# Kernel tuning notes

Measured on AMD Instinct MI355X. Metric: run time of the kernel, lower is better.

## Reference

```python
import jax, jax.numpy as jnp
import numpy as np

DIM = 768
HEADS = 12
HD = DIM // HEADS  # 64
BASE = 100.0


def rope_sincos(H, W):
    # DINOv3 RopePositionEmbedding: normalize_coords='separate', base=100.0
    dd = HD // 4
    periods = BASE ** (jnp.arange(dd, dtype=jnp.float32) / dd)          # [dd]
    ch = (jnp.arange(H, dtype=jnp.float32) + 0.5) / H                    # pixel centers
    cw = (jnp.arange(W, dtype=jnp.float32) + 0.5) / W
    cy, cx = jnp.meshgrid(ch, cw, indexing='ij')
    coords = 2.0 * jnp.stack([cy, cx], axis=-1).reshape(H * W, 2) - 1.0  # [N,2] in [-1,1]
    angles = 2.0 * jnp.pi * coords[:, :, None] / periods[None, None, :]  # [N,2,dd]
    angles = angles.reshape(H * W, 2 * dd)                               # [N, HD//2]
    angles = jnp.concatenate([angles, angles], axis=-1)                  # [N, HD]
    return jnp.sin(angles), jnp.cos(angles)


def rotate_half(t):
    t1, t2 = jnp.split(t, 2, axis=-1)
    return jnp.concatenate([-t2, t1], axis=-1)


def setup_inputs() -> dict:
    key = jax.random.key(0)
    k1, k2, k3 = jax.random.split(key, 3)
    B, H, W = 2, 48, 48
    x = jax.random.normal(k1, (B, H, W, DIM), dtype=jnp.float32)
    w_qkv = jax.random.normal(k2, (3 * DIM, DIM), dtype=jnp.float32) * 0.02
    b_qkv = jnp.zeros((3 * DIM,), dtype=jnp.float32)
    w_proj = jax.random.normal(k3, (DIM, DIM), dtype=jnp.float32) * 0.02
    b_proj = jnp.zeros((DIM,), dtype=jnp.float32)
    return {"x": x, "w_qkv": w_qkv, "b_qkv": b_qkv, "w_proj": w_proj, "b_proj": b_proj}


def reference(x, w_qkv, b_qkv, w_proj, b_proj):
    B, H, W, C = x.shape
    N = H * W
    xf = x.reshape(B, N, C)
    qkv = xf @ w_qkv.T + b_qkv                                   # [B,N,3C]
    qkv = qkv.reshape(B, N, 3, HEADS, HD).transpose(2, 0, 3, 1, 4)
    q, k, v = qkv[0], qkv[1], qkv[2]                              # [B,h,N,d]
    sin, cos = rope_sincos(H, W)                                  # [N,d]
    q = q * cos + rotate_half(q) * sin
    k = k * cos + rotate_half(k) * sin
    scale = HD ** -0.5
    attn = jax.nn.softmax(jnp.einsum('bhqd,bhkd->bhqk', q, k) * scale, axis=-1)
    o = jnp.einsum('bhqk,bhkd->bhqd', attn, v)                    # [B,h,N,d]
    o = o.transpose(0, 2, 1, 3).reshape(B, N, C)
    o = o @ w_proj.T + b_proj
    return o.reshape(B, H, W, C)
```

## Files before the change

kernel.cpp:

```cpp
#include <hip/hip_runtime.h>

#define BATCH 2
#define NSEQ 2304
#define DIM 768
#define HEADS 12
#define HD 64
#define M_TOK (BATCH * NSEQ)
#define LDSP 72
#define KP 72
#define BH (BATCH * HEADS)
#define KT_HALF (NSEQ / 64 / 2)

typedef __attribute__((ext_vector_type(8))) short bf16x8;
typedef __attribute__((ext_vector_type(8))) short short8v;
typedef __attribute__((ext_vector_type(4))) float f32x4;
typedef __fp16 fp16x2 __attribute__((ext_vector_type(2)));
typedef _Float16 half4 __attribute__((ext_vector_type(4)));
typedef _Float16 half8 __attribute__((ext_vector_type(8)));

#define QSCALE (0.125f * 1.44269504088896f)
#define LOG2_100_D16 0.41524101186092029f

__device__ __forceinline__ short f2bf(float f) {
    union { float f; unsigned u; } v; v.f = f;
    unsigned r = v.u + 0x7fffu + ((v.u >> 16) & 1u);
    return (short)(r >> 16);
}

#define CN1 (M_TOK * DIM / 4)
#define CN2 (3 * DIM * DIM / 4)
#define CN3 (DIM * DIM / 4)
__global__ void cvt_all_kernel(const float* __restrict__ x, const float* __restrict__ wq,
                               const float* __restrict__ wp,
                               short* __restrict__ xb, short* __restrict__ wqb,
                               short* __restrict__ wpb) {
    int i = blockIdx.x * 256 + threadIdx.x;
    const float* src; short* dst; int j;
    if (i < CN1)              { src = x;  dst = xb;  j = i; }
    else if (i < CN1 + CN2)   { src = wq; dst = wqb; j = i - CN1; }
    else                      { src = wp; dst = wpb; j = i - CN1 - CN2; }
    float4 v = reinterpret_cast<const float4*>(src)[j];
    short4 o;
    o.x = f2bf(v.x); o.y = f2bf(v.y); o.z = f2bf(v.z); o.w = f2bf(v.w);
    reinterpret_cast<short4*>(dst)[j] = o;
}

__global__ __launch_bounds__(256) void gemm_qkv_kernel(
    const short* __restrict__ A,
    const short* __restrict__ Bt,
    const float* __restrict__ bias,
    short* __restrict__ qb, short* __restrict__ kbuf, _Float16* __restrict__ vtb)
{
    __shared__ __align__(16) short At[2][128 * LDSP];
    __shared__ __align__(16) short Bl[2][128 * LDSP];
    const int m0 = blockIdx.x * 128, n0 = blockIdx.y * 128;
    const int tid = threadIdx.x, lane = tid & 63, wave = tid >> 6;
    const int quad = lane >> 4, l16 = lane & 15;
    const int wm = (wave >> 1) * 64, wn = (wave & 1) * 64;
    const int r = tid >> 1, c0 = (tid & 1) * 32;
    f32x4 acc[4][4] = {};

    {
        const uint4* ga = reinterpret_cast<const uint4*>(&A[(size_t)(m0 + r) * DIM + c0]);
        const uint4* gb = reinterpret_cast<const uint4*>(&Bt[(size_t)(n0 + r) * DIM + c0]);
        uint4 a0 = ga[0], a1 = ga[1], a2 = ga[2], a3 = ga[3];
        uint4 b0 = gb[0], b1 = gb[1], b2 = gb[2], b3 = gb[3];
        uint4* sa = reinterpret_cast<uint4*>(&At[0][r * LDSP + c0]);
        uint4* sb = reinterpret_cast<uint4*>(&Bl[0][r * LDSP + c0]);
        sa[0] = a0; sa[1] = a1; sa[2] = a2; sa[3] = a3;
        sb[0] = b0; sb[1] = b1; sb[2] = b2; sb[3] = b3;
    }

    int cur = 0;
    for (int k0 = 0; k0 < DIM; k0 += 64) {
        __syncthreads();
        uint4 a0, a1, a2, a3, b0, b1, b2, b3;
        const bool pre = (k0 + 64 < DIM);
        if (pre) {
            const uint4* ga = reinterpret_cast<const uint4*>(&A[(size_t)(m0 + r) * DIM + k0 + 64 + c0]);
            const uint4* gb = reinterpret_cast<const uint4*>(&Bt[(size_t)(n0 + r) * DIM + k0 + 64 + c0]);
            a0 = ga[0]; a1 = ga[1]; a2 = ga[2]; a3 = ga[3];
            b0 = gb[0]; b1 = gb[1]; b2 = gb[2]; b3 = gb[3];
        }
#pragma unroll
        for (int ks = 0; ks < 2; ++ks) {
            bf16x8 af[4], bf[4];
#pragma unroll
            for (int mt = 0; mt < 4; ++mt)
                af[mt] = *reinterpret_cast<const bf16x8*>(&At[cur][(wm + mt * 16 + l16) * LDSP + ks * 32 + quad * 8]);
#pragma unroll
            for (int nt = 0; nt < 4; ++nt)
                bf[nt] = *reinterpret_cast<const bf16x8*>(&Bl[cur][(wn + nt * 16 + l16) * LDSP + ks * 32 + quad * 8]);
#pragma unroll
            for (int mt = 0; mt < 4; ++mt)
#pragma unroll
                for (int nt = 0; nt < 4; ++nt)
                    acc[mt][nt] = __builtin_amdgcn_mfma_f32_16x16x32_bf16(af[mt], bf[nt], acc[mt][nt], 0, 0, 0);
        }
        if (pre) {
            uint4* sa = reinterpret_cast<uint4*>(&At[cur ^ 1][r * LDSP + c0]);
            uint4* sb = reinterpret_cast<uint4*>(&Bl[cur ^ 1][r * LDSP + c0]);
            sa[0] = a0; sa[1] = a1; sa[2] = a2; sa[3] = a3;
            sb[0] = b0; sb[1] = b1; sb[2] = b2; sb[3] = b3;
        }
        cur ^= 1;
    }

    const int which = (n0 + wn) / DIM;
    const int head = ((n0 + wn) % DIM) / HD;
    const int b = m0 / NSEQ;
    const int tokb = m0 % NSEQ + wm;
    if (which == 2) {
#pragma unroll
        for (int mt = 0; mt < 4; ++mt)
#pragma unroll
            for (int nt = 0; nt < 4; ++nt) {
                const int n = n0 + wn + nt * 16 + l16;
                const int d = nt * 16 + l16;
                const float bi = bias[n];
                const int tok0 = tokb + mt * 16 + quad * 4;
                half4 hv;
                hv.x = (_Float16)(acc[mt][nt][0] + bi);
                hv.y = (_Float16)(acc[mt][nt][1] + bi);
                hv.z = (_Float16)(acc[mt][nt][2] + bi);
                hv.w = (_Float16)(acc[mt][nt][3] + bi);
                *reinterpret_cast<half4*>(&vtb[((size_t)(b * HEADS + head) * HD + d) * NSEQ + tok0]) = hv;
            }
    } else {
        short* dst = (which == 0) ? qb : kbuf;
        const float qs = (which == 0) ? QSCALE : 1.0f;
        float bi[4];
#pragma unroll
        for (int nt = 0; nt < 4; ++nt) bi[nt] = bias[n0 + wn + nt * 16 + l16];
        const float invp = __builtin_amdgcn_exp2f(-(float)l16 * LOG2_100_D16);
#pragma unroll
        for (int mt = 0; mt < 4; ++mt) {
#pragma unroll
            for (int rg = 0; rg < 4; ++rg) {
                const int tok = tokb + mt * 16 + quad * 4 + rg;
                const int yy = tok / 48, xx = tok - yy * 48;
                const float ry = (2.0f * (yy + 0.5f) * (1.0f / 48.0f) - 1.0f) * invp;
                const float rx = (2.0f * (xx + 0.5f) * (1.0f / 48.0f) - 1.0f) * invp;
                const float sy = __builtin_amdgcn_sinf(ry), cy = __builtin_amdgcn_cosf(ry);
                const float sx = __builtin_amdgcn_sinf(rx), cx = __builtin_amdgcn_cosf(rx);
                const float a0 = acc[mt][0][rg] + bi[0];
                const float a1 = acc[mt][1][rg] + bi[1];
                const float a2 = acc[mt][2][rg] + bi[2];
                const float a3 = acc[mt][3][rg] + bi[3];
                short* rp = &dst[((size_t)(b * HEADS + head) * NSEQ + tok) * HD];
                rp[l16]      = f2bf((a0 * cy - a2 * sy) * qs);
                rp[32 + l16] = f2bf((a2 * cy + a0 * sy) * qs);
                rp[16 + l16] = f2bf((a1 * cx - a3 * sx) * qs);
                rp[48 + l16] = f2bf((a3 * cx + a1 * sx) * qs);
            }
        }
    }
}

__global__ __launch_bounds__(256, 2) void attn_kernel(
    const short* __restrict__ qb, const short* __restrict__ kb,
    const _Float16* __restrict__ vtb, _Float16* __restrict__ opart,
    float* __restrict__ lpart)
{
    __shared__ __align__(16) short    Kt[2][64 * KP];
    __shared__ __align__(16) _Float16 Vt[2][64 * KP];
    const int wg = blockIdx.x;
    const int xcd = wg & 7;
    const int slot = wg >> 3;
    const int slab = xcd * 6 + slot / 9;
    const int qt = slot % 9;
    const int kh = slab & 1;
    const int bh = slab >> 1;
    const int tid = threadIdx.x, lane = tid & 63, wave = tid >> 6;
    const int quad = lane >> 4, l16 = lane & 15;
    const int qrow0 = qt * 256 + wave * 64;
    const short* qbase = qb + (size_t)bh * NSEQ * HD;
    const short* kbase = kb + (size_t)bh * NSEQ * HD;
    const _Float16* vbase = vtb + (size_t)bh * HD * NSEQ;

    bf16x8 qf[4][2];
#pragma unroll
    for (int mt = 0; mt < 4; ++mt)
#pragma unroll
        for (int ks = 0; ks < 2; ++ks)
            qf[mt][ks] = *reinterpret_cast<const bf16x8*>(
                &qbase[(size_t)(qrow0 + mt * 16 + l16) * HD + ks * 32 + quad * 8]);

    half4 ones;
    ones.x = ones.y = ones.z = ones.w = (_Float16)1.0f;

    f32x4 oacc[4][4] = {};
    f32x4 lacc[4] = {};

    const int r = tid >> 2, cq = (tid & 3) * 16;
    const int t0 = kh * KT_HALF;
    const short* kp = kbase + (size_t)(t0 * 64 + r) * HD + cq;
    const _Float16* vp = vbase + (size_t)r * NSEQ + t0 * 64 + cq;
    {
        const uint4* gk = reinterpret_cast<const uint4*>(kp);
        uint4 k0 = gk[0], k1 = gk[1];
        const uint4* gv = reinterpret_cast<const uint4*>(vp);
        uint4 v0 = gv[0], v1 = gv[1];
        uint4* sk = reinterpret_cast<uint4*>(&Kt[0][r * KP + cq]);
        sk[0] = k0; sk[1] = k1;
        uint4* sv = reinterpret_cast<uint4*>(&Vt[0][r * KP + cq]);
        sv[0] = v0; sv[1] = v1;
        kp += 64 * HD;
        vp += 64;
    }

    int cur = 0;
    for (int kt = 0; kt < KT_HALF; ++kt) {
        __syncthreads();
        uint4 k0, k1, v0, v1;
        const bool pre = (kt + 1 < KT_HALF);
        if (pre) {
            const uint4* gk = reinterpret_cast<const uint4*>(kp);
            k0 = gk[0]; k1 = gk[1];
            const uint4* gv = reinterpret_cast<const uint4*>(vp);
            v0 = gv[0]; v1 = gv[1];
            kp += 64 * HD;
            vp += 64;
        }

        bf16x8 kf[2][4];
#pragma unroll
        for (int ks = 0; ks < 2; ++ks)
#pragma unroll
            for (int nt = 0; nt < 4; ++nt)
                kf[ks][nt] = *reinterpret_cast<const bf16x8*>(
                    &Kt[cur][(nt * 16 + l16) * KP + ks * 32 + quad * 8]);
        half4 vf[4][4];
#pragma unroll
        for (int nt = 0; nt < 4; ++nt)
#pragma unroll
            for (int dt = 0; dt < 4; ++dt)
                vf[nt][dt] = *reinterpret_cast<const half4*>(
                    &Vt[cur][(dt * 16 + l16) * KP + nt * 16 + quad * 4]);

#pragma unroll
        for (int mt = 0; mt < 4; ++mt) {
            f32x4 sacc[4] = {};
#pragma unroll
            for (int ks = 0; ks < 2; ++ks)
#pragma unroll
                for (int nt = 0; nt < 4; ++nt)
                    sacc[nt] = __builtin_amdgcn_mfma_f32_16x16x32_bf16(
                        kf[ks][nt], qf[mt][ks], sacc[nt], 0, 0, 0);

            half4 pf[4];
#pragma unroll
            for (int nt = 0; nt < 4; ++nt) {
                fp16x2 lo = __builtin_amdgcn_cvt_pkrtz(
                    __builtin_amdgcn_exp2f(sacc[nt][0]),
                    __builtin_amdgcn_exp2f(sacc[nt][1]));
                fp16x2 hi = __builtin_amdgcn_cvt_pkrtz(
                    __builtin_amdgcn_exp2f(sacc[nt][2]),
                    __builtin_amdgcn_exp2f(sacc[nt][3]));
                half4 p;
                p.x = (_Float16)lo.x; p.y = (_Float16)lo.y;
                p.z = (_Float16)hi.x; p.w = (_Float16)hi.y;
                pf[nt] = p;
            }

#pragma unroll
            for (int nt = 0; nt < 4; ++nt)
                lacc[mt] = __builtin_amdgcn_mfma_f32_16x16x16f16(
                    pf[nt], ones, lacc[mt], 0, 0, 0);
#pragma unroll
            for (int nt = 0; nt < 4; ++nt)
#pragma unroll
                for (int dt = 0; dt < 4; ++dt)
                    oacc[mt][dt] = __builtin_amdgcn_mfma_f32_16x16x16f16(
                        pf[nt], vf[nt][dt], oacc[mt][dt], 0, 0, 0);
        }

        if (pre) {
            uint4* sk = reinterpret_cast<uint4*>(&Kt[cur ^ 1][r * KP + cq]);
            sk[0] = k0; sk[1] = k1;
            uint4* sv = reinterpret_cast<uint4*>(&Vt[cur ^ 1][r * KP + cq]);
            sv[0] = v0; sv[1] = v1;
        }
        cur ^= 1;
    }

    _Float16* ob2 = opart + (size_t)(kh * BH + bh) * NSEQ * HD;
    float* lp2 = lpart + (size_t)(kh * BH + bh) * NSEQ;
#pragma unroll
    for (int mt = 0; mt < 4; ++mt) {
#pragma unroll
        for (int dt = 0; dt < 4; ++dt)
#pragma unroll
            for (int rg = 0; rg < 4; ++rg) {
                int row = qrow0 + mt * 16 + quad * 4 + rg;
                ob2[(size_t)row * HD + dt * 16 + l16] = (_Float16)oacc[mt][dt][rg];
            }
        if (l16 == 0) {
#pragma unroll
            for (int rg = 0; rg < 4; ++rg)
                lp2[qrow0 + mt * 16 + quad * 4 + rg] = lacc[mt][rg];
        }
    }
}

__global__ __launch_bounds__(256) void gemm_proj_kernel(
    const _Float16* __restrict__ op,
    const float* __restrict__ lp,
    const short* __restrict__ Bt,
    const float* __restrict__ bias,
    float* __restrict__ out)
{
    __shared__ __align__(16) short At[64 * LDSP];
    __shared__ __align__(16) short Bl[64 * LDSP];
    const int m0 = blockIdx.x * 64, n0 = blockIdx.y * 64;
    const int tid = threadIdx.x, lane = tid & 63, wave = tid >> 6;
    const int quad = lane >> 4, l16 = lane & 15;
    const int wm = (wave >> 1) * 32, wn = (wave & 1) * 32;
    const int r = tid >> 2, cs = (tid & 3) * 16;
    const int b = m0 / NSEQ;
    const int tok = m0 % NSEQ + r;
    f32x4 acc[2][2] = {};

    for (int k0 = 0; k0 < DIM; k0 += 64) {
        const int h = k0 >> 6;
        const size_t pb = (size_t)(b * HEADS + h) * NSEQ + tok;
        const float l0 = lp[pb], l1 = lp[(size_t)BH * NSEQ + pb];
        const float inv = __builtin_amdgcn_rcpf(l0 + l1);
        const half8* o0 = reinterpret_cast<const half8*>(&op[pb * HD + cs]);
        const half8* o1 = reinterpret_cast<const half8*>(&op[(size_t)BH * NSEQ * HD + pb * HD + cs]);
        half8 p0 = o0[0], p1 = o0[1], q0 = o1[0], q1 = o1[1];
        const uint4* gb = reinterpret_cast<const uint4*>(&Bt[(size_t)(n0 + r) * DIM + k0 + cs]);
        uint4 bw0 = gb[0], bw1 = gb[1];
        short8v s0, s1;
#pragma unroll
        for (int j = 0; j < 8; ++j) {
            s0[j] = f2bf(((float)p0[j] + (float)q0[j]) * inv);
            s1[j] = f2bf(((float)p1[j] + (float)q1[j]) * inv);
        }
        *reinterpret_cast<short8v*>(&At[r * LDSP + cs]) = s0;
        *reinterpret_cast<short8v*>(&At[r * LDSP + cs + 8]) = s1;
        uint4* sb = reinterpret_cast<uint4*>(&Bl[r * LDSP + cs]);
        sb[0] = bw0; sb[1] = bw1;
        __syncthreads();
#pragma unroll
        for (int ks = 0; ks < 2; ++ks) {
            bf16x8 af[2], bf[2];
#pragma unroll
            for (int mt = 0; mt < 2; ++mt)
                af[mt] = *reinterpret_cast<const bf16x8*>(&At[(wm + mt * 16 + l16) * LDSP + ks * 32 + quad * 8]);
#pragma unroll
            for (int nt = 0; nt < 2; ++nt)
                bf[nt] = *reinterpret_cast<const bf16x8*>(&Bl[(wn + nt * 16 + l16) * LDSP + ks * 32 + quad * 8]);
#pragma unroll
            for (int mt = 0; mt < 2; ++mt)
#pragma unroll
                for (int nt = 0; nt < 2; ++nt)
                    acc[mt][nt] = __builtin_amdgcn_mfma_f32_16x16x32_bf16(af[mt], bf[nt], acc[mt][nt], 0, 0, 0);
        }
        __syncthreads();
    }

#pragma unroll
    for (int mt = 0; mt < 2; ++mt)
#pragma unroll
        for (int nt = 0; nt < 2; ++nt) {
            const int n = n0 + wn + nt * 16 + l16;
            const float bi = bias[n];
#pragma unroll
            for (int rg = 0; rg < 4; ++rg) {
                const int m = m0 + wm + mt * 16 + quad * 4 + rg;
                out[(size_t)m * DIM + n] = acc[mt][nt][rg] + bi;
            }
        }
}

extern "C" void kernel_launch(void* const* d_in, const int* in_sizes, int n_in,
                              void* d_out, int out_size, void* d_ws, size_t ws_size,
                              hipStream_t stream) {
    const float* x      = (const float*)d_in[0];
    const float* w_qkv  = (const float*)d_in[1];
    const float* b_qkv  = (const float*)d_in[2];
    const float* w_proj = (const float*)d_in[3];
    const float* b_proj = (const float*)d_in[4];
    float* out = (float*)d_out;

    short* xb     = (short*)d_ws;
    short* wqkvb  = xb + (size_t)M_TOK * DIM;
    short* wprojb = wqkvb + (size_t)3 * DIM * DIM;
    short* qb     = wprojb + (size_t)DIM * DIM;
    short* kb     = qb + (size_t)BH * NSEQ * HD;
    short* vtb    = kb + (size_t)BH * NSEQ * HD;
    short* opart  = vtb + (size_t)BH * NSEQ * HD;
    float* lpart  = (float*)(opart + (size_t)2 * BH * NSEQ * HD);

    cvt_all_kernel<<<(CN1 + CN2 + CN3) / 256, 256, 0, stream>>>(
        x, w_qkv, w_proj, xb, wqkvb, wprojb);

    dim3 g1(M_TOK / 128, 3 * DIM / 128);
    gemm_qkv_kernel<<<g1, 256, 0, stream>>>(xb, wqkvb, b_qkv, qb, kb, (_Float16*)vtb);

    attn_kernel<<<dim3(9 * 2 * BH), 256, 0, stream>>>(qb, kb, (const _Float16*)vtb,
                                                      (_Float16*)opart, lpart);

    dim3 g3(M_TOK / 64, DIM / 64);
    gemm_proj_kernel<<<g3, 256, 0, stream>>>((const _Float16*)opart, lpart,
                                             wprojb, b_proj, out);
}
```

Before: 173.4 us.

## Fuse fp32-to-bf16 conversion into GEMM loads and enlarge proj tiles

Removes the standalone conversion kernel and converts x, w_qkv and w_proj to bf16 while staging tiles into shared memory in the QKV and projection GEMMs. This eliminates one launch and the write and re-read of bf16 copies in the workspace. The projection GEMM tile grows from 64x64 to 128x128 with a 4x4 MFMA accumulator per wave. In exchange, GEMMs read fp32 (double bytes per tile), weights are re-converted by every block, and the proj grid shrinks to fewer blocks, with higher register pressure.

New measurement: 251.1 us. 44.8% more time.

```diff
diff --git a/kernel.cpp b/kernel.cpp
--- a/kernel.cpp
+++ b/kernel.cpp
@@ -27,27 +27,14 @@
     return (short)(r >> 16);
 }
 
-#define CN1 (M_TOK * DIM / 4)
-#define CN2 (3 * DIM * DIM / 4)
-#define CN3 (DIM * DIM / 4)
-__global__ void cvt_all_kernel(const float* __restrict__ x, const float* __restrict__ wq,
-                               const float* __restrict__ wp,
-                               short* __restrict__ xb, short* __restrict__ wqb,
-                               short* __restrict__ wpb) {
-    int i = blockIdx.x * 256 + threadIdx.x;
-    const float* src; short* dst; int j;
-    if (i < CN1)              { src = x;  dst = xb;  j = i; }
-    else if (i < CN1 + CN2)   { src = wq; dst = wqb; j = i - CN1; }
-    else                      { src = wp; dst = wpb; j = i - CN1 - CN2; }
-    float4 v = reinterpret_cast<const float4*>(src)[j];
-    short4 o;
-    o.x = f2bf(v.x); o.y = f2bf(v.y); o.z = f2bf(v.z); o.w = f2bf(v.w);
-    reinterpret_cast<short4*>(dst)[j] = o;
+__device__ __forceinline__ void cvt8(const float4& lo, const float4& hi, short8v& s) {
+    s[0] = f2bf(lo.x); s[1] = f2bf(lo.y); s[2] = f2bf(lo.z); s[3] = f2bf(lo.w);
+    s[4] = f2bf(hi.x); s[5] = f2bf(hi.y); s[6] = f2bf(hi.z); s[7] = f2bf(hi.w);
 }
 
 __global__ __launch_bounds__(256) void gemm_qkv_kernel(
-    const short* __restrict__ A,
-    const short* __restrict__ Bt,
+    const float* __restrict__ A,
+    const float* __restrict__ Bt,
     const float* __restrict__ bias,
     short* __restrict__ qb, short* __restrict__ kbuf, _Float16* __restrict__ vtb)
 {
@@ -57,30 +44,35 @@
     const int tid = threadIdx.x, lane = tid & 63, wave = tid >> 6;
     const int quad = lane >> 4, l16 = lane & 15;
     const int wm = (wave >> 1) * 64, wn = (wave & 1) * 64;
-    const int r = tid >> 1, c0 = (tid & 1) * 32;
+    const int r = tid >> 1, c0e = (tid & 1) * 32;
     f32x4 acc[4][4] = {};
 
     {
-        const uint4* ga = reinterpret_cast<const uint4*>(&A[(size_t)(m0 + r) * DIM + c0]);
-        const uint4* gb = reinterpret_cast<const uint4*>(&Bt[(size_t)(n0 + r) * DIM + c0]);
-        uint4 a0 = ga[0], a1 = ga[1], a2 = ga[2], a3 = ga[3];
-        uint4 b0 = gb[0], b1 = gb[1], b2 = gb[2], b3 = gb[3];
-        uint4* sa = reinterpret_cast<uint4*>(&At[0][r * LDSP + c0]);
-        uint4* sb = reinterpret_cast<uint4*>(&Bl[0][r * LDSP + c0]);
-        sa[0] = a0; sa[1] = a1; sa[2] = a2; sa[3] = a3;
-        sb[0] = b0; sb[1] = b1; sb[2] = b2; sb[3] = b3;
+        const float4* ga = reinterpret_cast<const float4*>(&A[(size_t)(m0 + r) * DIM + c0e]);
+        const float4* gb = reinterpret_cast<const float4*>(&Bt[(size_t)(n0 + r) * DIM + c0e]);
+        float4 av[8], bv[8];
+#pragma unroll
+        for (int j = 0; j < 8; ++j) { av[j] = ga[j]; bv[j] = gb[j]; }
+#pragma unroll
+        for (int c = 0; c < 4; ++c) {
+            short8v sa, sb;
+            cvt8(av[2 * c], av[2 * c + 1], sa);
+            cvt8(bv[2 * c], bv[2 * c + 1], sb);
+            *reinterpret_cast<short8v*>(&At[0][r * LDSP + c0e + c * 8]) = sa;
+            *reinterpret_cast<short8v*>(&Bl[0][r * LDSP + c0e + c * 8]) = sb;
+        }
     }
 
     int cur = 0;
     for (int k0 = 0; k0 < DIM; k0 += 64) {
         __syncthreads();
-        uint4 a0, a1, a2, a3, b0, b1, b2, b3;
+        float4 av[8], bv[8];
         const bool pre = (k0 + 64 < DIM);
         if (pre) {
-            const uint4* ga = reinterpret_cast<const uint4*>(&A[(size_t)(m0 + r) * DIM + k0 + 64 + c0]);
-            const uint4* gb = reinterpret_cast<const uint4*>(&Bt[(size_t)(n0 + r) * DIM + k0 + 64 + c0]);
-            a0 = ga[0]; a1 = ga[1]; a2 = ga[2]; a3 = ga[3];
-            b0 = gb[0]; b1 = gb[1]; b2 = gb[2]; b3 = gb[3];
+            const float4* ga = reinterpret_cast<const float4*>(&A[(size_t)(m0 + r) * DIM + k0 + 64 + c0e]);
+            const float4* gb = reinterpret_cast<const float4*>(&Bt[(size_t)(n0 + r) * DIM + k0 + 64 + c0e]);
+#pragma unroll
+            for (int j = 0; j < 8; ++j) { av[j] = ga[j]; bv[j] = gb[j]; }
         }
 #pragma unroll
         for (int ks = 0; ks < 2; ++ks) {
@@ -98,10 +90,14 @@
                     acc[mt][nt] = __builtin_amdgcn_mfma_f32_16x16x32_bf16(af[mt], bf[nt], acc[mt][nt], 0, 0, 0);
         }
         if (pre) {
-            uint4* sa = reinterpret_cast<uint4*>(&At[cur ^ 1][r * LDSP + c0]);
-            uint4* sb = reinterpret_cast<uint4*>(&Bl[cur ^ 1][r * LDSP + c0]);
-            sa[0] = a0; sa[1] = a1; sa[2] = a2; sa[3] = a3;
-            sb[0] = b0; sb[1] = b1; sb[2] = b2; sb[3] = b3;
+#pragma unroll
+            for (int c = 0; c < 4; ++c) {
+                short8v sa, sb;
+                cvt8(av[2 * c], av[2 * c + 1], sa);
+                cvt8(bv[2 * c], bv[2 * c + 1], sb);
+                *reinterpret_cast<short8v*>(&At[cur ^ 1][r * LDSP + c0e + c * 8]) = sa;
+                *reinterpret_cast<short8v*>(&Bl[cur ^ 1][r * LDSP + c0e + c * 8]) = sb;
+            }
         }
         cur ^= 1;
     }
@@ -306,64 +302,75 @@
 __global__ __launch_bounds__(256) void gemm_proj_kernel(
     const _Float16* __restrict__ op,
     const float* __restrict__ lp,
-    const short* __restrict__ Bt,
+    const float* __restrict__ Bt,
     const float* __restrict__ bias,
     float* __restrict__ out)
 {
-    __shared__ __align__(16) short At[64 * LDSP];
-    __shared__ __align__(16) short Bl[64 * LDSP];
-    const int m0 = blockIdx.x * 64, n0 = blockIdx.y * 64;
+    __shared__ __align__(16) short At[128 * LDSP];
+    __shared__ __align__(16) short Bl[128 * LDSP];
+    const int m0 = blockIdx.x * 128, n0 = blockIdx.y * 128;
     const int tid = threadIdx.x, lane = tid & 63, wave = tid >> 6;
     const int quad = lane >> 4, l16 = lane & 15;
-    const int wm = (wave >> 1) * 32, wn = (wave & 1) * 32;
-    const int r = tid >> 2, cs = (tid & 3) * 16;
+    const int wm = (wave >> 1) * 64, wn = (wave & 1) * 64;
+    const int r = tid >> 1, c0e = (tid & 1) * 32;
     const int b = m0 / NSEQ;
     const int tok = m0 % NSEQ + r;
-    f32x4 acc[2][2] = {};
+    f32x4 acc[4][4] = {};
 
     for (int k0 = 0; k0 < DIM; k0 += 64) {
         const int h = k0 >> 6;
         const size_t pb = (size_t)(b * HEADS + h) * NSEQ + tok;
         const float l0 = lp[pb], l1 = lp[(size_t)BH * NSEQ + pb];
         const float inv = __builtin_amdgcn_rcpf(l0 + l1);
-        const half8* o0 = reinterpret_cast<const half8*>(&op[pb * HD + cs]);
-        const half8* o1 = reinterpret_cast<const half8*>(&op[(size_t)BH * NSEQ * HD + pb * HD + cs]);
-        half8 p0 = o0[0], p1 = o0[1], q0 = o1[0], q1 = o1[1];
-        const uint4* gb = reinterpret_cast<const uint4*>(&Bt[(size_t)(n0 + r) * DIM + k0 + cs]);
-        uint4 bw0 = gb[0], bw1 = gb[1];
-        short8v s0, s1;
+        const half8* o0 = reinterpret_cast<const half8*>(&op[pb * HD + c0e]);
+        const half8* o1 = reinterpret_cast<const half8*>(&op[(size_t)BH * NSEQ * HD + pb * HD + c0e]);
+        half8 p0 = o0[0], p1 = o0[1], p2 = o0[2], p3 = o0[3];
+        half8 q0 = o1[0], q1 = o1[1], q2 = o1[2], q3 = o1[3];
+        const float4* gb = reinterpret_cast<const float4*>(&Bt[(size_t)(n0 + r) * DIM + k0 + c0e]);
+        float4 bv[8];
+#pragma unroll
+        for (int j = 0; j < 8; ++j) bv[j] = gb[j];
+        short8v s0, s1, s2, s3;
 #pragma unroll
         for (int j = 0; j < 8; ++j) {
             s0[j] = f2bf(((float)p0[j] + (float)q0[j]) * inv);
             s1[j] = f2bf(((float)p1[j] + (float)q1[j]) * inv);
-        }
-        *reinterpret_cast<short8v*>(&At[r * LDSP + cs]) = s0;
-        *reinterpret_cast<short8v*>(&At[r * LDSP + cs + 8]) = s1;
-        uint4* sb = reinterpret_cast<uint4*>(&Bl[r * LDSP + cs]);
-        sb[0] = bw0; sb[1] = bw1;
+            s2[j] = f2bf(((float)p2[j] + (float)q2[j]) * inv);
+            s3[j] = f2bf(((float)p3[j] + (float)q3[j]) * inv);
+        }
+        *reinterpret_cast<short8v*>(&At[r * LDSP + c0e])      = s0;
+        *reinterpret_cast<short8v*>(&At[r * LDSP + c0e + 8])  = s1;
+        *reinterpret_cast<short8v*>(&At[r * LDSP + c0e + 16]) = s2;
+        *reinterpret_cast<short8v*>(&At[r * LDSP + c0e + 24]) = s3;
+#pragma unroll
+        for (int c = 0; c < 4; ++c) {
+            short8v sb;
+            cvt8(bv[2 * c], bv[2 * c + 1], sb);
+            *reinterpret_cast<short8v*>(&Bl[r * LDSP + c0e + c * 8]) = sb;
+        }
         __syncthreads();
 #pragma unroll
         for (int ks = 0; ks < 2; ++ks) {
-            bf16x8 af[2], bf[2];
-#pragma unroll
-            for (int mt = 0; mt < 2; ++mt)
+            bf16x8 af[4], bf[4];
+#pragma unroll
+            for (int mt = 0; mt < 4; ++mt)
                 af[mt] = *reinterpret_cast<const bf16x8*>(&At[(wm + mt * 16 + l16) * LDSP + ks * 32 + quad * 8]);
 #pragma unroll
-            for (int nt = 0; nt < 2; ++nt)
+            for (int nt = 0; nt < 4; ++nt)
                 bf[nt] = *reinterpret_cast<const bf16x8*>(&Bl[(wn + nt * 16 + l16) * LDSP + ks * 32 + quad * 8]);
 #pragma unroll
-            for (int mt = 0; mt < 2; ++mt)
-#pragma unroll
-                for (int nt = 0; nt < 2; ++nt)
+            for (int mt = 0; mt < 4; ++mt)
+#pragma unroll
+                for (int nt = 0; nt < 4; ++nt)
                     acc[mt][nt] = __builtin_amdgcn_mfma_f32_16x16x32_bf16(af[mt], bf[nt], acc[mt][nt], 0, 0, 0);
         }
         __syncthreads();
     }
 
 #pragma unroll
-    for (int mt = 0; mt < 2; ++mt)
-#pragma unroll
-        for (int nt = 0; nt < 2; ++nt) {
+    for (int mt = 0; mt < 4; ++mt)
+#pragma unroll
+        for (int nt = 0; nt < 4; ++nt) {
             const int n = n0 + wn + nt * 16 + l16;
             const float bi = bias[n];
 #pragma unroll
@@ -384,25 +391,19 @@
     const float* b_proj = (const float*)d_in[4];
     float* out = (float*)d_out;
 
-    short* xb     = (short*)d_ws;
-    short* wqkvb  = xb + (size_t)M_TOK * DIM;
-    short* wprojb = wqkvb + (size_t)3 * DIM * DIM;
-    short* qb     = wprojb + (size_t)DIM * DIM;
+    short* qb     = (short*)d_ws;
     short* kb     = qb + (size_t)BH * NSEQ * HD;
     short* vtb    = kb + (size_t)BH * NSEQ * HD;
     short* opart  = vtb + (size_t)BH * NSEQ * HD;
     float* lpart  = (float*)(opart + (size_t)2 * BH * NSEQ * HD);
 
-    cvt_all_kernel<<<(CN1 + CN2 + CN3) / 256, 256, 0, stream>>>(
-        x, w_qkv, w_proj, xb, wqkvb, wprojb);
-
     dim3 g1(M_TOK / 128, 3 * DIM / 128);
-    gemm_qkv_kernel<<<g1, 256, 0, stream>>>(xb, wqkvb, b_qkv, qb, kb, (_Float16*)vtb);
+    gemm_qkv_kernel<<<g1, 256, 0, stream>>>(x, w_qkv, b_qkv, qb, kb, (_Float16*)vtb);
 
     attn_kernel<<<dim3(9 * 2 * BH), 256, 0, stream>>>(qb, kb, (const _Float16*)vtb,
                                                       (_Float16*)opart, lpart);
 
-    dim3 g3(M_TOK / 64, DIM / 64);
+    dim3 g3(M_TOK / 128, DIM / 128);
     gemm_proj_kernel<<<g3, 256, 0, stream>>>((const _Float16*)opart, lpart,
-                                             wprojb, b_proj, out);
-}
+                                             w_proj, b_proj, out);
+}
```
